# Optimization experiments

Hardware: AMD Instinct MI355X
Metric: run time of the kernel (lower is better)

Reference implementation:

```python
import jax, jax.numpy as jnp
import numpy as np

LN_EPS = 1e-5

def _layernorm(x, g, b):
    m = jnp.mean(x, axis=-1, keepdims=True)
    v = jnp.mean((x - m) ** 2, axis=-1, keepdims=True)
    return (x - m) / jnp.sqrt(v + LN_EPS) * g + b

def _mlp(x, w1, g1, b1, w2, g2, b2):
    # Linear(no bias) -> LayerNorm -> Linear(no bias) -> LayerNorm -> ReLU
    x = _layernorm(x @ w1, g1, b1)
    x = _layernorm(x @ w2, g2, b2)
    return jax.nn.relu(x)

def setup_inputs() -> dict:
    key = jax.random.key(0)
    ks = jax.random.split(key, 16)
    Lc, Lf, N, Dc, Df, K = 1024, 4096, 32, 256, 128, 8
    inv = lambda d: 1.0 / np.sqrt(d)
    inp = {
        "features_coarse": jax.random.normal(ks[0], (Lc, N, Dc), dtype=jnp.float32),
        "features_fine": jax.random.normal(ks[1], (Lf, N, Df), dtype=jnp.float32),
        # mlp_coarse: d_in=Dc, d_ff=Df, d_out=Df
        "w1c": jax.random.uniform(ks[2], (Dc, Df), jnp.float32, -inv(Dc), inv(Dc)),
        "g1c": jnp.ones((Df,), jnp.float32),
        "b1c": jnp.zeros((Df,), jnp.float32),
        "w2c": jax.random.uniform(ks[3], (Df, Df), jnp.float32, -inv(Df), inv(Df)),
        "g2c": jnp.ones((Df,), jnp.float32),
        "b2c": jnp.zeros((Df,), jnp.float32),
        # mlp_fine: d_in=Df, d_ff=Df, d_out=Df
        "w1f": jax.random.uniform(ks[4], (Df, Df), jnp.float32, -inv(Df), inv(Df)),
        "g1f": jnp.ones((Df,), jnp.float32),
        "b1f": jnp.zeros((Df,), jnp.float32),
        "w2f": jax.random.uniform(ks[5], (Df, Df), jnp.float32, -inv(Df), inv(Df)),
        "g2f": jnp.ones((Df,), jnp.float32),
        "b2f": jnp.zeros((Df,), jnp.float32),
        "neighbor_row": jax.random.randint(ks[6], (K * Lc * N,), 0, Lf, dtype=jnp.int64 if jax.config.jax_enable_x64 else jnp.int32),
        "neighbor_col": jax.random.randint(ks[7], (K * Lc * N,), 0, N, dtype=jnp.int64 if jax.config.jax_enable_x64 else jnp.int32),
        "keep_idx": jax.random.randint(ks[8], (Lc,), 0, Lf, dtype=jnp.int64 if jax.config.jax_enable_x64 else jnp.int32),
    }
    return inp

def reference(features_coarse, features_fine, w1c, g1c, b1c, w2c, g2c, b2c,
              w1f, g1f, b1f, w2f, g2f, b2f, neighbor_row, neighbor_col, keep_idx):
    Lc, N, Dc = features_coarse.shape
    Lf, _, Df = features_fine.shape
    D = Df
    fc = _mlp(features_coarse, w1c, g1c, b1c, w2c, g2c, b2c)  # (Lc, N, D)
    ff = _mlp(features_fine, w1f, g1f, b1f, w2f, g2f, b2f)    # (Lf, N, D)
    gathered = ff[neighbor_row, neighbor_col]                  # (K*Lc*N, D)
    updated = fc[None] + gathered.reshape(-1, Lc, N, D)        # (K, Lc, N, D)
    ff = ff.at[neighbor_row, neighbor_col].set(updated.reshape(-1, D))
    return ff
```

## Files before the change

### kernel.cpp

```cpp
#include <hip/hip_runtime.h>
#include <hip/hip_bf16.h>

typedef __attribute__((ext_vector_type(8))) short s8v;
typedef __attribute__((ext_vector_type(4))) float f4v;

__device__ __forceinline__ short f2bf(float f) {
    __hip_bfloat16 h = __float2bfloat16(f);
    union { __hip_bfloat16 h; short s; } u{h};
    return u.s;
}
__device__ __forceinline__ float bf2f(unsigned short v) {
    union { unsigned u; float f; } x; x.u = ((unsigned)v) << 16; return x.f;
}
__device__ __forceinline__ unsigned packbf(float a, float b) {
    return (unsigned)(unsigned short)f2bf(a) | ((unsigned)(unsigned short)f2bf(b) << 16);
}

__global__ void prep_kernel(const float* __restrict__ w1c, const float* __restrict__ w2c,
                            const float* __restrict__ g1c, const float* __restrict__ b1c,
                            const float* __restrict__ w1f, const float* __restrict__ w2f,
                            const float* __restrict__ g1f, const float* __restrict__ b1f,
                            short* __restrict__ p1c, short* __restrict__ p2c,
                            short* __restrict__ p1f, short* __restrict__ p2f,
                            float* __restrict__ s2c, float* __restrict__ bwc,
                            float* __restrict__ s2f, float* __restrict__ bwf,
                            int* __restrict__ win)
{
    int b = blockIdx.x, t = threadIdx.x;
    if (b >= 42) {
        int idx4 = (b - 42) * 256 + t;
        int4 z; z.x = 0; z.y = 0; z.z = 0; z.w = 0;
        *(int4*)(win + idx4 * 4) = z;
        return;
    }
    if (b >= 40) {
        if (t >= 128) return;
        const float* W  = (b == 40) ? w2c : w2f;
        const float* g1 = (b == 40) ? g1c : g1f;
        const float* b1 = (b == 40) ? b1c : b1f;
        float* s2 = (b == 40) ? s2c : s2f;
        float* bw = (b == 40) ? bwc : bwf;
        float s = 0.f, w2sum = 0.f;
        for (int k = 0; k < 128; ++k) {
            float wv = W[k * 128 + t];
            s     += bf2f((unsigned short)f2bf(g1[k] * wv));
            w2sum += b1[k] * wv;
        }
        s2[t] = s; bw[t] = w2sum;
        return;
    }
    int id = b * 256 + t;
    int f  = id >> 6, l = id & 63;
    const float* W; const float* g1 = nullptr; short* P; int fl;
    if      (f < 64)  { W = w1c; P = p1c; fl = f; }
    else if (f < 96)  { W = w2c; P = p2c; fl = f - 64;  g1 = g1c; }
    else if (f < 128) { W = w1f; P = p1f; fl = f - 96; }
    else              { W = w2f; P = p2f; fl = f - 128; g1 = g1f; }
    int g = l >> 4, c = l & 15;
    int ks = fl >> 3, n = fl & 7;
    s8v o;
    #pragma unroll
    for (int e = 0; e < 8; ++e) {
        int k = ks*32 + g*8 + e;
        float v = W[k * 128 + n*16 + c];
        if (g1) v *= g1[k];
        o[e] = f2bf(v);
    }
    *(s8v*)(P + ((fl*64 + l) << 3)) = o;
}

template<int K1, bool FINE>
__global__ __launch_bounds__(512, 4)
void mlp_mfma(const float* __restrict__ X,
              const short* __restrict__ WpA,
              const short* __restrict__ WpB,
              const float* __restrict__ s2v, const float* __restrict__ bwv,
              const float* __restrict__ g2v, const float* __restrict__ b2v,
              float* __restrict__ outF,
              unsigned short* __restrict__ outB,
              const int* __restrict__ winner,
              const unsigned short* __restrict__ fcB,
              const int* __restrict__ nr, const int* __restrict__ nc,
              int* __restrict__ win, int nWinBlocks)
{
    __shared__ short Ws[32768];
    constexpr int W2OFF = (K1 == 128) ? 16384 : 0;

    if (blockIdx.x < (unsigned)nWinBlocks) {
        int i = blockIdx.x * 512 + threadIdx.x;
        atomicMax(&win[nr[i] * 32 + nc[i]], i + 1);
        return;
    }
    const int bid  = blockIdx.x - nWinBlocks;
    const int tid  = threadIdx.x;
    const int wave = tid >> 6, lane = tid & 63;
    const int G = lane >> 4, n16 = lane & 15;
    const int row = bid * 128 + wave * 16 + n16;
    const size_t rowK = (size_t)row * K1;

    int wv = 0;
    if constexpr (FINE) wv = winner[row];

    #pragma unroll
    for (int r = 0; r < (K1 == 128 ? 4 : 8); ++r) {
        int ch = r*512 + tid;
        *(s8v*)&Ws[ch*8] = *(const s8v*)(WpA + (size_t)ch*8);
    }
    if constexpr (K1 == 128) {
        #pragma unroll
        for (int r = 0; r < 4; ++r) {
            int ch = r*512 + tid;
            *(s8v*)&Ws[16384 + ch*8] = *(const s8v*)(WpB + (size_t)ch*8);
        }
    }

    const float* pX = X + rowK + G*8;
    float4 aPf[4][2];
    #pragma unroll
    for (int k2 = 0; k2 < 4; ++k2) {
        aPf[k2][0] = *(const float4*)(pX + k2*32);
        aPf[k2][1] = *(const float4*)(pX + k2*32 + 4);
    }

    ushort4 gv[8];
    bool hasw = false;
    if constexpr (FINE) {
        hasw = (wv > 0);
        const size_t src = (size_t)((wv - 1) & 32767) * 128;
        if (hasw) {
            #pragma unroll
            for (int mt = 0; mt < 8; ++mt)
                gv[mt] = *(const ushort4*)(fcB + src + mt*16 + G*4);
        }
    }

    __syncthreads();

    f4v acc1[8];
    #pragma unroll
    for (int mt = 0; mt < 8; ++mt) acc1[mt] = (f4v){0.f, 0.f, 0.f, 0.f};

    #pragma unroll
    for (int kb = 0; kb < K1/32; kb += 4) {
        #pragma unroll
        for (int k2 = 0; k2 < 4; ++k2) {
            const int ks = kb + k2;
            s8v wfr[8];
            #pragma unroll
            for (int mt = 0; mt < 8; ++mt)
                wfr[mt] = *(const s8v*)&Ws[((ks*8 + mt)*64 + lane) * 8];
            s8v xf;
            xf[0] = f2bf(aPf[k2][0].x); xf[1] = f2bf(aPf[k2][0].y);
            xf[2] = f2bf(aPf[k2][0].z); xf[3] = f2bf(aPf[k2][0].w);
            xf[4] = f2bf(aPf[k2][1].x); xf[5] = f2bf(aPf[k2][1].y);
            xf[6] = f2bf(aPf[k2][1].z); xf[7] = f2bf(aPf[k2][1].w);
            #pragma unroll
            for (int mt = 0; mt < 8; ++mt)
                acc1[mt] = __builtin_amdgcn_mfma_f32_16x16x32_bf16(wfr[mt], xf, acc1[mt], 0, 0, 0);
        }
        if (kb + 4 < K1/32) {
            #pragma unroll
            for (int k2 = 0; k2 < 4; ++k2) {
                aPf[k2][0] = *(const float4*)(pX + (kb+4+k2)*32);
                aPf[k2][1] = *(const float4*)(pX + (kb+4+k2)*32 + 4);
            }
        }
    }

    if constexpr (K1 == 256) {
        __syncthreads();
        #pragma unroll
        for (int r = 0; r < 4; ++r) {
            int ch = r*512 + tid;
            *(s8v*)&Ws[ch*8] = *(const s8v*)(WpB + (size_t)ch*8);
        }
        __syncthreads();
    }

    float sm = 0.f, sq = 0.f;
    #pragma unroll
    for (int mt = 0; mt < 8; ++mt)
        #pragma unroll
        for (int j = 0; j < 4; ++j) { float v = acc1[mt][j]; sm += v; sq += v*v; }
    sm += __shfl_xor(sm, 16, 64); sm += __shfl_xor(sm, 32, 64);
    sq += __shfl_xor(sq, 16, 64); sq += __shfl_xor(sq, 32, 64);
    const float mean1 = sm * (1.f/128.f);
    const float rstd1 = rsqrtf(sq * (1.f/128.f) - mean1*mean1 + 1e-5f);

    unsigned pk[8][2];
    #pragma unroll
    for (int mt = 0; mt < 8; ++mt) {
        pk[mt][0] = packbf(acc1[mt][0], acc1[mt][1]);
        pk[mt][1] = packbf(acc1[mt][2], acc1[mt][3]);
    }

    f4v acc2[8];
    #pragma unroll
    for (int mt = 0; mt < 8; ++mt) acc2[mt] = (f4v){0.f, 0.f, 0.f, 0.f};

    const int src0 = ((G & 1) << 5) + n16;
    const int src1 = src0 + 16;
    const bool hiG = (G >= 2);
    #pragma unroll
    for (int ks = 0; ks < 4; ++ks) {
        int r00 = __shfl((int)pk[2*ks][0],   src0, 64);
        int r01 = __shfl((int)pk[2*ks][1],   src0, 64);
        int r02 = __shfl((int)pk[2*ks][0],   src1, 64);
        int r03 = __shfl((int)pk[2*ks][1],   src1, 64);
        int r10 = __shfl((int)pk[2*ks+1][0], src0, 64);
        int r11 = __shfl((int)pk[2*ks+1][1], src0, 64);
        int r12 = __shfl((int)pk[2*ks+1][0], src1, 64);
        int r13 = __shfl((int)pk[2*ks+1][1], src1, 64);
        union { int u[4]; s8v v; } hb;
        hb.u[0] = hiG ? r10 : r00; hb.u[1] = hiG ? r11 : r01;
        hb.u[2] = hiG ? r12 : r02; hb.u[3] = hiG ? r13 : r03;
        s8v wfr[8];
        #pragma unroll
        for (int mt = 0; mt < 8; ++mt)
            wfr[mt] = *(const s8v*)&Ws[W2OFF + ((ks*8 + mt)*64 + lane) * 8];
        #pragma unroll
        for (int mt = 0; mt < 8; ++mt)
            acc2[mt] = __builtin_amdgcn_mfma_f32_16x16x32_bf16(wfr[mt], hb.v, acc2[mt], 0, 0, 0);
    }

    float h2[8][4];
    float sm2 = 0.f, sq2 = 0.f;
    #pragma unroll
    for (int mt = 0; mt < 8; ++mt) {
        const int col = mt*16 + G*4;
        f4v s2l = *(const f4v*)&s2v[col];
        f4v bwl = *(const f4v*)&bwv[col];
        #pragma unroll
        for (int j = 0; j < 4; ++j) {
            float v = rstd1 * (acc2[mt][j] - mean1 * s2l[j]) + bwl[j];
            h2[mt][j] = v; sm2 += v; sq2 += v*v;
        }
    }
    sm2 += __shfl_xor(sm2, 16, 64); sm2 += __shfl_xor(sm2, 32, 64);
    sq2 += __shfl_xor(sq2, 16, 64); sq2 += __shfl_xor(sq2, 32, 64);
    const float mean2 = sm2 * (1.f/128.f);
    const float rstd2 = rsqrtf(sq2 * (1.f/128.f) - mean2*mean2 + 1e-5f);

    if constexpr (FINE) {
        #pragma unroll
        for (int mt = 0; mt < 8; ++mt) {
            const int col = mt*16 + G*4;
            f4v g2l = *(const f4v*)&g2v[col];
            f4v b2l = *(const f4v*)&b2v[col];
            float z0 = fmaxf((h2[mt][0]-mean2)*rstd2*g2l[0] + b2l[0], 0.f);
            float z1 = fmaxf((h2[mt][1]-mean2)*rstd2*g2l[1] + b2l[1], 0.f);
            float z2 = fmaxf((h2[mt][2]-mean2)*rstd2*g2l[2] + b2l[2], 0.f);
            float z3 = fmaxf((h2[mt][3]-mean2)*rstd2*g2l[3] + b2l[3], 0.f);
            if (hasw) {
                z0 += bf2f(gv[mt].x); z1 += bf2f(gv[mt].y);
                z2 += bf2f(gv[mt].z); z3 += bf2f(gv[mt].w);
            }
            float4 o; o.x = z0; o.y = z1; o.z = z2; o.w = z3;
            *(float4*)(outF + (size_t)row * 128 + col) = o;
        }
    } else {
        #pragma unroll
        for (int mt = 0; mt < 8; ++mt) {
            const int col = mt*16 + G*4;
            f4v g2l = *(const f4v*)&g2v[col];
            f4v b2l = *(const f4v*)&b2v[col];
            ushort4 o;
            o.x = (unsigned short)f2bf(fmaxf((h2[mt][0]-mean2)*rstd2*g2l[0] + b2l[0], 0.f));
            o.y = (unsigned short)f2bf(fmaxf((h2[mt][1]-mean2)*rstd2*g2l[1] + b2l[1], 0.f));
            o.z = (unsigned short)f2bf(fmaxf((h2[mt][2]-mean2)*rstd2*g2l[2] + b2l[2], 0.f));
            o.w = (unsigned short)f2bf(fmaxf((h2[mt][3]-mean2)*rstd2*g2l[3] + b2l[3], 0.f));
            *(ushort4*)(outB + (size_t)row * 128 + col) = o;
        }
    }
}

extern "C" void kernel_launch(void* const* d_in, const int* in_sizes, int n_in,
                              void* d_out, int out_size, void* d_ws, size_t ws_size,
                              hipStream_t stream)
{
    const float* fcoarse = (const float*)d_in[0];
    const float* ffine   = (const float*)d_in[1];
    const float* w1c = (const float*)d_in[2];
    const float* g1c = (const float*)d_in[3];
    const float* b1c = (const float*)d_in[4];
    const float* w2c = (const float*)d_in[5];
    const float* g2c = (const float*)d_in[6];
    const float* b2c = (const float*)d_in[7];
    const float* w1f = (const float*)d_in[8];
    const float* g1f = (const float*)d_in[9];
    const float* b1f = (const float*)d_in[10];
    const float* w2f = (const float*)d_in[11];
    const float* g2f = (const float*)d_in[12];
    const float* b2f = (const float*)d_in[13];
    const int* nrow  = (const int*)d_in[14];
    const int* ncol  = (const int*)d_in[15];

    float* out = (float*)d_out;
    const int Mc = 32768, Mf = 131072;

    unsigned short* fcB = (unsigned short*)d_ws;
    char* base = (char*)d_ws;
    int*   winner = (int*)(base + 8u*1024*1024);
    short* p1c = (short*)(base + 8u*1024*1024 + 512u*1024);
    short* p2c = p1c + 256*128;
    short* p1f = p2c + 128*128;
    short* p2f = p1f + 128*128;
    float* s2c = (float*)(p2f + 128*128);
    float* bwc = s2c + 128;
    float* s2f = bwc + 128;
    float* bwf = s2f + 128;

    prep_kernel<<<170, 256, 0, stream>>>(w1c, w2c, g1c, b1c, w1f, w2f, g1f, b1f,
                                         p1c, p2c, p1f, p2f, s2c, bwc, s2f, bwf,
                                         winner);

    mlp_mfma<256, false><<<512 + Mc/128, 512, 0, stream>>>(
        fcoarse, p1c, p2c, s2c, bwc, g2c, b2c,
        nullptr, fcB, nullptr, nullptr,
        nrow, ncol, winner, 512);

    mlp_mfma<128, true><<<Mf/128, 512, 0, stream>>>(
        ffine, p1f, p2f, s2f, bwf, g2f, b2f,
        out, nullptr, winner, fcB,
        nullptr, nullptr, nullptr, 0);
}
```

Baseline: 74.35 us.

## Process multiple row tiles per block with prefetch and keep both weight matrices resident in LDS

The MLP kernel now loops over NT row tiles per block, loading weights into LDS once and prefetching the next tile's inputs and winner index while computing the current one. The fine pass uses two tiles per block with half the grid. The coarse pass keeps W1 and W2 together in a larger LDS buffer instead of reloading W2 between the two GEMMs, which drops two barriers. The aim is to amortize weight staging and hide global load latency, at the cost of more LDS per block (96KB for coarse), which may reduce occupancy.

```diff
diff --git a/kernel.cpp b/kernel.cpp
--- a/kernel.cpp
+++ b/kernel.cpp
@@ -69,7 +69,7 @@
     *(s8v*)(P + ((fl*64 + l) << 3)) = o;
 }
 
-template<int K1, bool FINE>
+template<int K1, bool FINE, int NT>
 __global__ __launch_bounds__(512, 4)
 void mlp_mfma(const float* __restrict__ X,
               const short* __restrict__ WpA,
@@ -83,8 +83,9 @@
               const int* __restrict__ nr, const int* __restrict__ nc,
               int* __restrict__ win, int nWinBlocks)
 {
-    __shared__ short Ws[32768];
-    constexpr int W2OFF = (K1 == 128) ? 16384 : 0;
+    __shared__ short Ws[(K1 == 256) ? 49152 : 32768];
+    constexpr int W2OFF = (K1 == 256) ? 32768 : 16384;
+    constexpr int NCH1  = (K1/32) * 8 * 64;
 
     if (blockIdx.x < (unsigned)nWinBlocks) {
         int i = blockIdx.x * 512 + threadIdx.x;
@@ -95,182 +96,211 @@
     const int tid  = threadIdx.x;
     const int wave = tid >> 6, lane = tid & 63;
     const int G = lane >> 4, n16 = lane & 15;
-    const int row = bid * 128 + wave * 16 + n16;
-    const size_t rowK = (size_t)row * K1;
-
-    int wv = 0;
-    if constexpr (FINE) wv = winner[row];
+    const int row0 = bid * NT * 128 + wave * 16 + n16;
 
     #pragma unroll
-    for (int r = 0; r < (K1 == 128 ? 4 : 8); ++r) {
+    for (int r = 0; r < NCH1/512; ++r) {
         int ch = r*512 + tid;
         *(s8v*)&Ws[ch*8] = *(const s8v*)(WpA + (size_t)ch*8);
     }
-    if constexpr (K1 == 128) {
-        #pragma unroll
-        for (int r = 0; r < 4; ++r) {
-            int ch = r*512 + tid;
-            *(s8v*)&Ws[16384 + ch*8] = *(const s8v*)(WpB + (size_t)ch*8);
-        }
-    }
-
-    const float* pX = X + rowK + G*8;
+    #pragma unroll
+    for (int r = 0; r < 4; ++r) {
+        int ch = r*512 + tid;
+        *(s8v*)&Ws[W2OFF + ch*8] = *(const s8v*)(WpB + (size_t)ch*8);
+    }
+
     float4 aPf[4][2];
+    {
+        const float* pX0 = X + (size_t)row0 * K1 + G*8;
+        #pragma unroll
+        for (int k2 = 0; k2 < 4; ++k2) {
+            aPf[k2][0] = *(const float4*)(pX0 + k2*32);
+            aPf[k2][1] = *(const float4*)(pX0 + k2*32 + 4);
+        }
+    }
+    int wv = 0;
+    if constexpr (FINE) wv = winner[row0];
+
+    __syncthreads();
+
     #pragma unroll
-    for (int k2 = 0; k2 < 4; ++k2) {
-        aPf[k2][0] = *(const float4*)(pX + k2*32);
-        aPf[k2][1] = *(const float4*)(pX + k2*32 + 4);
-    }
-
-    ushort4 gv[8];
-    bool hasw = false;
-    if constexpr (FINE) {
-        hasw = (wv > 0);
-        const size_t src = (size_t)((wv - 1) & 32767) * 128;
-        if (hasw) {
-            #pragma unroll
-            for (int mt = 0; mt < 8; ++mt)
-                gv[mt] = *(const ushort4*)(fcB + src + mt*16 + G*4);
-        }
-    }
-
-    __syncthreads();
-
-    f4v acc1[8];
-    #pragma unroll
-    for (int mt = 0; mt < 8; ++mt) acc1[mt] = (f4v){0.f, 0.f, 0.f, 0.f};
-
-    #pragma unroll
-    for (int kb = 0; kb < K1/32; kb += 4) {
+    for (int t = 0; t < NT; ++t) {
+        const int row = row0 + t*128;
+
+        s8v xf[4];
         #pragma unroll
         for (int k2 = 0; k2 < 4; ++k2) {
-            const int ks = kb + k2;
+            s8v v;
+            v[0] = f2bf(aPf[k2][0].x); v[1] = f2bf(aPf[k2][0].y);
+            v[2] = f2bf(aPf[k2][0].z); v[3] = f2bf(aPf[k2][0].w);
+            v[4] = f2bf(aPf[k2][1].x); v[5] = f2bf(aPf[k2][1].y);
+            v[6] = f2bf(aPf[k2][1].z); v[7] = f2bf(aPf[k2][1].w);
+            xf[k2] = v;
+        }
+
+        float4 bPf[4][2];
+        if constexpr (K1 == 256) {
+            const float* pX = X + (size_t)row * K1 + G*8;
+            #pragma unroll
+            for (int k2 = 0; k2 < 4; ++k2) {
+                bPf[k2][0] = *(const float4*)(pX + (4+k2)*32);
+                bPf[k2][1] = *(const float4*)(pX + (4+k2)*32 + 4);
+            }
+        }
+
+        int wv_next = 0;
+        if (t + 1 < NT) {
+            const float* pXn = X + (size_t)(row + 128) * K1 + G*8;
+            #pragma unroll
+            for (int k2 = 0; k2 < 4; ++k2) {
+                aPf[k2][0] = *(const float4*)(pXn + k2*32);
+                aPf[k2][1] = *(const float4*)(pXn + k2*32 + 4);
+            }
+            if constexpr (FINE) wv_next = winner[row + 128];
+        }
+
+        ushort4 gv[8];
+        bool hasw = false;
+        if constexpr (FINE) {
+            hasw = (wv > 0);
+            const size_t src = (size_t)((wv - 1) & 32767) * 128;
+            if (hasw) {
+                #pragma unroll
+                for (int mt = 0; mt < 8; ++mt)
+                    gv[mt] = *(const ushort4*)(fcB + src + mt*16 + G*4);
+            }
+        }
+
+        f4v acc[8];
+        #pragma unroll
+        for (int mt = 0; mt < 8; ++mt) acc[mt] = (f4v){0.f, 0.f, 0.f, 0.f};
+
+        #pragma unroll
+        for (int ks = 0; ks < 4; ++ks) {
             s8v wfr[8];
             #pragma unroll
             for (int mt = 0; mt < 8; ++mt)
                 wfr[mt] = *(const s8v*)&Ws[((ks*8 + mt)*64 + lane) * 8];
-            s8v xf;
-            xf[0] = f2bf(aPf[k2][0].x); xf[1] = f2bf(aPf[k2][0].y);
-            xf[2] = f2bf(aPf[k2][0].z); xf[3] = f2bf(aPf[k2][0].w);
-            xf[4] = f2bf(aPf[k2][1].x); xf[5] = f2bf(aPf[k2][1].y);
-            xf[6] = f2bf(aPf[k2][1].z); xf[7] = f2bf(aPf[k2][1].w);
             #pragma unroll
             for (int mt = 0; mt < 8; ++mt)
-                acc1[mt] = __builtin_amdgcn_mfma_f32_16x16x32_bf16(wfr[mt], xf, acc1[mt], 0, 0, 0);
-        }
-        if (kb + 4 < K1/32) {
+                acc[mt] = __builtin_amdgcn_mfma_f32_16x16x32_bf16(wfr[mt], xf[ks], acc[mt], 0, 0, 0);
+        }
+        if constexpr (K1 == 256) {
             #pragma unroll
             for (int k2 = 0; k2 < 4; ++k2) {
-                aPf[k2][0] = *(const float4*)(pX + (kb+4+k2)*32);
-                aPf[k2][1] = *(const float4*)(pX + (kb+4+k2)*32 + 4);
-            }
-        }
-    }
-
-    if constexpr (K1 == 256) {
-        __syncthreads();
-        #pragma unroll
-        for (int r = 0; r < 4; ++r) {
-            int ch = r*512 + tid;
-            *(s8v*)&Ws[ch*8] = *(const s8v*)(WpB + (size_t)ch*8);
-        }
-        __syncthreads();
-    }
-
-    float sm = 0.f, sq = 0.f;
-    #pragma unroll
-    for (int mt = 0; mt < 8; ++mt)
-        #pragma unroll
-        for (int j = 0; j < 4; ++j) { float v = acc1[mt][j]; sm += v; sq += v*v; }
-    sm += __shfl_xor(sm, 16, 64); sm += __shfl_xor(sm, 32, 64);
-    sq += __shfl_xor(sq, 16, 64); sq += __shfl_xor(sq, 32, 64);
-    const float mean1 = sm * (1.f/128.f);
-    const float rstd1 = rsqrtf(sq * (1.f/128.f) - mean1*mean1 + 1e-5f);
-
-    unsigned pk[8][2];
-    #pragma unroll
-    for (int mt = 0; mt < 8; ++mt) {
-        pk[mt][0] = packbf(acc1[mt][0], acc1[mt][1]);
-        pk[mt][1] = packbf(acc1[mt][2], acc1[mt][3]);
-    }
-
-    f4v acc2[8];
-    #pragma unroll
-    for (int mt = 0; mt < 8; ++mt) acc2[mt] = (f4v){0.f, 0.f, 0.f, 0.f};
-
-    const int src0 = ((G & 1) << 5) + n16;
-    const int src1 = src0 + 16;
-    const bool hiG = (G >= 2);
-    #pragma unroll
-    for (int ks = 0; ks < 4; ++ks) {
-        int r00 = __shfl((int)pk[2*ks][0],   src0, 64);
-        int r01 = __shfl((int)pk[2*ks][1],   src0, 64);
-        int r02 = __shfl((int)pk[2*ks][0],   src1, 64);
-        int r03 = __shfl((int)pk[2*ks][1],   src1, 64);
-        int r10 = __shfl((int)pk[2*ks+1][0], src0, 64);
-        int r11 = __shfl((int)pk[2*ks+1][1], src0, 64);
-        int r12 = __shfl((int)pk[2*ks+1][0], src1, 64);
-        int r13 = __shfl((int)pk[2*ks+1][1], src1, 64);
-        union { int u[4]; s8v v; } hb;
-        hb.u[0] = hiG ? r10 : r00; hb.u[1] = hiG ? r11 : r01;
-        hb.u[2] = hiG ? r12 : r02; hb.u[3] = hiG ? r13 : r03;
-        s8v wfr[8];
+                s8v v;
+                v[0] = f2bf(bPf[k2][0].x); v[1] = f2bf(bPf[k2][0].y);
+                v[2] = f2bf(bPf[k2][0].z); v[3] = f2bf(bPf[k2][0].w);
+                v[4] = f2bf(bPf[k2][1].x); v[5] = f2bf(bPf[k2][1].y);
+                v[6] = f2bf(bPf[k2][1].z); v[7] = f2bf(bPf[k2][1].w);
+                xf[k2] = v;
+            }
+            #pragma unroll
+            for (int ks = 4; ks < 8; ++ks) {
+                s8v wfr[8];
+                #pragma unroll
+                for (int mt = 0; mt < 8; ++mt)
+                    wfr[mt] = *(const s8v*)&Ws[((ks*8 + mt)*64 + lane) * 8];
+                #pragma unroll
+                for (int mt = 0; mt < 8; ++mt)
+                    acc[mt] = __builtin_amdgcn_mfma_f32_16x16x32_bf16(wfr[mt], xf[ks-4], acc[mt], 0, 0, 0);
+            }
+        }
+
+        float sm = 0.f, sq = 0.f;
         #pragma unroll
         for (int mt = 0; mt < 8; ++mt)
-            wfr[mt] = *(const s8v*)&Ws[W2OFF + ((ks*8 + mt)*64 + lane) * 8];
-        #pragma unroll
-        for (int mt = 0; mt < 8; ++mt)
-            acc2[mt] = __builtin_amdgcn_mfma_f32_16x16x32_bf16(wfr[mt], hb.v, acc2[mt], 0, 0, 0);
-    }
-
-    float h2[8][4];
-    float sm2 = 0.f, sq2 = 0.f;
-    #pragma unroll
-    for (int mt = 0; mt < 8; ++mt) {
-        const int col = mt*16 + G*4;
-        f4v s2l = *(const f4v*)&s2v[col];
-        f4v bwl = *(const f4v*)&bwv[col];
-        #pragma unroll
-        for (int j = 0; j < 4; ++j) {
-            float v = rstd1 * (acc2[mt][j] - mean1 * s2l[j]) + bwl[j];
-            h2[mt][j] = v; sm2 += v; sq2 += v*v;
-        }
-    }
-    sm2 += __shfl_xor(sm2, 16, 64); sm2 += __shfl_xor(sm2, 32, 64);
-    sq2 += __shfl_xor(sq2, 16, 64); sq2 += __shfl_xor(sq2, 32, 64);
-    const float mean2 = sm2 * (1.f/128.f);
-    const float rstd2 = rsqrtf(sq2 * (1.f/128.f) - mean2*mean2 + 1e-5f);
-
-    if constexpr (FINE) {
+            #pragma unroll
+            for (int j = 0; j < 4; ++j) { float v = acc[mt][j]; sm += v; sq += v*v; }
+        sm += __shfl_xor(sm, 16, 64); sm += __shfl_xor(sm, 32, 64);
+        sq += __shfl_xor(sq, 16, 64); sq += __shfl_xor(sq, 32, 64);
+        const float mean1 = sm * (1.f/128.f);
+        const float rstd1 = rsqrtf(sq * (1.f/128.f) - mean1*mean1 + 1e-5f);
+
+        unsigned pk[8][2];
+        #pragma unroll
+        for (int mt = 0; mt < 8; ++mt) {
+            pk[mt][0] = packbf(acc[mt][0], acc[mt][1]);
+            pk[mt][1] = packbf(acc[mt][2], acc[mt][3]);
+            acc[mt] = (f4v){0.f, 0.f, 0.f, 0.f};
+        }
+
+        const int src0 = ((G & 1) << 5) + n16;
+        const int src1 = src0 + 16;
+        const bool hiG = (G >= 2);
+        #pragma unroll
+        for (int ks = 0; ks < 4; ++ks) {
+            int r00 = __shfl((int)pk[2*ks][0],   src0, 64);
+            int r01 = __shfl((int)pk[2*ks][1],   src0, 64);
+            int r02 = __shfl((int)pk[2*ks][0],   src1, 64);
+            int r03 = __shfl((int)pk[2*ks][1],   src1, 64);
+            int r10 = __shfl((int)pk[2*ks+1][0], src0, 64);
+            int r11 = __shfl((int)pk[2*ks+1][1], src0, 64);
+            int r12 = __shfl((int)pk[2*ks+1][0], src1, 64);
+            int r13 = __shfl((int)pk[2*ks+1][1], src1, 64);
+            union { int u[4]; s8v v; } hb;
+            hb.u[0] = hiG ? r10 : r00; hb.u[1] = hiG ? r11 : r01;
+            hb.u[2] = hiG ? r12 : r02; hb.u[3] = hiG ? r13 : r03;
+            s8v wfr[8];
+            #pragma unroll
+            for (int mt = 0; mt < 8; ++mt)
+                wfr[mt] = *(const s8v*)&Ws[W2OFF + ((ks*8 + mt)*64 + lane) * 8];
+            #pragma unroll
+            for (int mt = 0; mt < 8; ++mt)
+                acc[mt] = __builtin_amdgcn_mfma_f32_16x16x32_bf16(wfr[mt], hb.v, acc[mt], 0, 0, 0);
+        }
+
+        float h2[8][4];
+        float sm2 = 0.f, sq2 = 0.f;
         #pragma unroll
         for (int mt = 0; mt < 8; ++mt) {
             const int col = mt*16 + G*4;
-            f4v g2l = *(const f4v*)&g2v[col];
-            f4v b2l = *(const f4v*)&b2v[col];
-            float z0 = fmaxf((h2[mt][0]-mean2)*rstd2*g2l[0] + b2l[0], 0.f);
-            float z1 = fmaxf((h2[mt][1]-mean2)*rstd2*g2l[1] + b2l[1], 0.f);
-            float z2 = fmaxf((h2[mt][2]-mean2)*rstd2*g2l[2] + b2l[2], 0.f);
-            float z3 = fmaxf((h2[mt][3]-mean2)*rstd2*g2l[3] + b2l[3], 0.f);
-            if (hasw) {
-                z0 += bf2f(gv[mt].x); z1 += bf2f(gv[mt].y);
-                z2 += bf2f(gv[mt].z); z3 += bf2f(gv[mt].w);
-            }
-            float4 o; o.x = z0; o.y = z1; o.z = z2; o.w = z3;
-            *(float4*)(outF + (size_t)row * 128 + col) = o;
-        }
-    } else {
-        #pragma unroll
-        for (int mt = 0; mt < 8; ++mt) {
-            const int col = mt*16 + G*4;
-            f4v g2l = *(const f4v*)&g2v[col];
-            f4v b2l = *(const f4v*)&b2v[col];
-            ushort4 o;
-            o.x = (unsigned short)f2bf(fmaxf((h2[mt][0]-mean2)*rstd2*g2l[0] + b2l[0], 0.f));
-            o.y = (unsigned short)f2bf(fmaxf((h2[mt][1]-mean2)*rstd2*g2l[1] + b2l[1], 0.f));
-            o.z = (unsigned short)f2bf(fmaxf((h2[mt][2]-mean2)*rstd2*g2l[2] + b2l[2], 0.f));
-            o.w = (unsigned short)f2bf(fmaxf((h2[mt][3]-mean2)*rstd2*g2l[3] + b2l[3], 0.f));
-            *(ushort4*)(outB + (size_t)row * 128 + col) = o;
-        }
+            f4v s2l = *(const f4v*)&s2v[col];
+            f4v bwl = *(const f4v*)&bwv[col];
+            #pragma unroll
+            for (int j = 0; j < 4; ++j) {
+                float v = rstd1 * (acc[mt][j] - mean1 * s2l[j]) + bwl[j];
+                h2[mt][j] = v; sm2 += v; sq2 += v*v;
+            }
+        }
+        sm2 += __shfl_xor(sm2, 16, 64); sm2 += __shfl_xor(sm2, 32, 64);
+        sq2 += __shfl_xor(sq2, 16, 64); sq2 += __shfl_xor(sq2, 32, 64);
+        const float mean2 = sm2 * (1.f/128.f);
+        const float rstd2 = rsqrtf(sq2 * (1.f/128.f) - mean2*mean2 + 1e-5f);
+
+        if constexpr (FINE) {
+            #pragma unroll
+            for (int mt = 0; mt < 8; ++mt) {
+                const int col = mt*16 + G*4;
+                f4v g2l = *(const f4v*)&g2v[col];
+                f4v b2l = *(const f4v*)&b2v[col];
+                float z0 = fmaxf((h2[mt][0]-mean2)*rstd2*g2l[0] + b2l[0], 0.f);
+                float z1 = fmaxf((h2[mt][1]-mean2)*rstd2*g2l[1] + b2l[1], 0.f);
+                float z2 = fmaxf((h2[mt][2]-mean2)*rstd2*g2l[2] + b2l[2], 0.f);
+                float z3 = fmaxf((h2[mt][3]-mean2)*rstd2*g2l[3] + b2l[3], 0.f);
+                if (hasw) {
+                    z0 += bf2f(gv[mt].x); z1 += bf2f(gv[mt].y);
+                    z2 += bf2f(gv[mt].z); z3 += bf2f(gv[mt].w);
+                }
+                float4 o; o.x = z0; o.y = z1; o.z = z2; o.w = z3;
+                *(float4*)(outF + (size_t)row * 128 + col) = o;
+            }
+        } else {
+            #pragma unroll
+            for (int mt = 0; mt < 8; ++mt) {
+                const int col = mt*16 + G*4;
+                f4v g2l = *(const f4v*)&g2v[col];
+                f4v b2l = *(const f4v*)&b2v[col];
+                ushort4 o;
+                o.x = (unsigned short)f2bf(fmaxf((h2[mt][0]-mean2)*rstd2*g2l[0] + b2l[0], 0.f));
+                o.y = (unsigned short)f2bf(fmaxf((h2[mt][1]-mean2)*rstd2*g2l[1] + b2l[1], 0.f));
+                o.z = (unsigned short)f2bf(fmaxf((h2[mt][2]-mean2)*rstd2*g2l[2] + b2l[2], 0.f));
+                o.w = (unsigned short)f2bf(fmaxf((h2[mt][3]-mean2)*rstd2*g2l[3] + b2l[3], 0.f));
+                *(ushort4*)(outB + (size_t)row * 128 + col) = o;
+            }
+        }
+
+        wv = wv_next;
     }
 }
 
@@ -314,12 +344,12 @@
                                          p1c, p2c, p1f, p2f, s2c, bwc, s2f, bwf,
                                          winner);
 
-    mlp_mfma<256, false><<<512 + Mc/128, 512, 0, stream>>>(
+    mlp_mfma<256, false, 1><<<512 + Mc/128, 512, 0, stream>>>(
         fcoarse, p1c, p2c, s2c, bwc, g2c, b2c,
         nullptr, fcB, nullptr, nullptr,
         nrow, ncol, winner, 512);
 
-    mlp_mfma<128, true><<<Mf/128, 512, 0, stream>>>(
+    mlp_mfma<128, true, 2><<<Mf/256, 512, 0, stream>>>(
         ffine, p1f, p2f, s2f, bwf, g2f, b2f,
         out, nullptr, winner, fcB,
         nullptr, nullptr, nullptr, 0);
```

Result: slower. 78.08 us (+5.0%).

## Stage fine MLP input and output through swizzled LDS for coalesced access

Applied to the files above, without the earlier changes.

Splits the templated MLP kernel into separate coarse and fine kernels. The fine kernel now loads its input rows cooperatively with coalesced float4 reads, converts them to bf16 and stores them in an XOR-swizzled shared buffer, in two halves so the second half's load overlaps the first half's MFMAs. The epilogue writes activations to shared memory as bf16 and reads them back so each lane writes 32 contiguous bytes per row, adding the gathered coarse contribution along the way. This targets uncoalesced global traffic, but it rounds the fine output to bf16 before the residual add and uses 16 KB more shared memory per block.

```diff
diff --git a/kernel.cpp b/kernel.cpp
--- a/kernel.cpp
+++ b/kernel.cpp
@@ -69,22 +69,16 @@
     *(s8v*)(P + ((fl*64 + l) << 3)) = o;
 }
 
-template<int K1, bool FINE>
 __global__ __launch_bounds__(512, 4)
-void mlp_mfma(const float* __restrict__ X,
-              const short* __restrict__ WpA,
-              const short* __restrict__ WpB,
-              const float* __restrict__ s2v, const float* __restrict__ bwv,
-              const float* __restrict__ g2v, const float* __restrict__ b2v,
-              float* __restrict__ outF,
-              unsigned short* __restrict__ outB,
-              const int* __restrict__ winner,
-              const unsigned short* __restrict__ fcB,
-              const int* __restrict__ nr, const int* __restrict__ nc,
-              int* __restrict__ win, int nWinBlocks)
+void coarse_mlp(const float* __restrict__ X,
+                const short* __restrict__ WpA, const short* __restrict__ WpB,
+                const float* __restrict__ s2v, const float* __restrict__ bwv,
+                const float* __restrict__ g2v, const float* __restrict__ b2v,
+                unsigned short* __restrict__ outB,
+                const int* __restrict__ nr, const int* __restrict__ nc,
+                int* __restrict__ win, int nWinBlocks)
 {
     __shared__ short Ws[32768];
-    constexpr int W2OFF = (K1 == 128) ? 16384 : 0;
 
     if (blockIdx.x < (unsigned)nWinBlocks) {
         int i = blockIdx.x * 512 + threadIdx.x;
@@ -93,25 +87,16 @@
     }
     const int bid  = blockIdx.x - nWinBlocks;
     const int tid  = threadIdx.x;
-    const int wave = tid >> 6, lane = tid & 63;
+    const int lane = tid & 63;
+    const int wave = tid >> 6;
     const int G = lane >> 4, n16 = lane & 15;
     const int row = bid * 128 + wave * 16 + n16;
-    const size_t rowK = (size_t)row * K1;
-
-    int wv = 0;
-    if constexpr (FINE) wv = winner[row];
-
-    #pragma unroll
-    for (int r = 0; r < (K1 == 128 ? 4 : 8); ++r) {
+    const size_t rowK = (size_t)row * 256;
+
+    #pragma unroll
+    for (int r = 0; r < 8; ++r) {
         int ch = r*512 + tid;
         *(s8v*)&Ws[ch*8] = *(const s8v*)(WpA + (size_t)ch*8);
-    }
-    if constexpr (K1 == 128) {
-        #pragma unroll
-        for (int r = 0; r < 4; ++r) {
-            int ch = r*512 + tid;
-            *(s8v*)&Ws[16384 + ch*8] = *(const s8v*)(WpB + (size_t)ch*8);
-        }
     }
 
     const float* pX = X + rowK + G*8;
@@ -121,19 +106,6 @@
         aPf[k2][0] = *(const float4*)(pX + k2*32);
         aPf[k2][1] = *(const float4*)(pX + k2*32 + 4);
     }
-
-    ushort4 gv[8];
-    bool hasw = false;
-    if constexpr (FINE) {
-        hasw = (wv > 0);
-        const size_t src = (size_t)((wv - 1) & 32767) * 128;
-        if (hasw) {
-            #pragma unroll
-            for (int mt = 0; mt < 8; ++mt)
-                gv[mt] = *(const ushort4*)(fcB + src + mt*16 + G*4);
-        }
-    }
-
     __syncthreads();
 
     f4v acc1[8];
@@ -141,7 +113,7 @@
     for (int mt = 0; mt < 8; ++mt) acc1[mt] = (f4v){0.f, 0.f, 0.f, 0.f};
 
     #pragma unroll
-    for (int kb = 0; kb < K1/32; kb += 4) {
+    for (int kb = 0; kb < 8; kb += 4) {
         #pragma unroll
         for (int k2 = 0; k2 < 4; ++k2) {
             const int ks = kb + k2;
@@ -158,7 +130,7 @@
             for (int mt = 0; mt < 8; ++mt)
                 acc1[mt] = __builtin_amdgcn_mfma_f32_16x16x32_bf16(wfr[mt], xf, acc1[mt], 0, 0, 0);
         }
-        if (kb + 4 < K1/32) {
+        if (kb + 4 < 8) {
             #pragma unroll
             for (int k2 = 0; k2 < 4; ++k2) {
                 aPf[k2][0] = *(const float4*)(pX + (kb+4+k2)*32);
@@ -167,15 +139,13 @@
         }
     }
 
-    if constexpr (K1 == 256) {
-        __syncthreads();
-        #pragma unroll
-        for (int r = 0; r < 4; ++r) {
-            int ch = r*512 + tid;
-            *(s8v*)&Ws[ch*8] = *(const s8v*)(WpB + (size_t)ch*8);
-        }
-        __syncthreads();
-    }
+    __syncthreads();
+    #pragma unroll
+    for (int r = 0; r < 4; ++r) {
+        int ch = r*512 + tid;
+        *(s8v*)&Ws[ch*8] = *(const s8v*)(WpB + (size_t)ch*8);
+    }
+    __syncthreads();
 
     float sm = 0.f, sq = 0.f;
     #pragma unroll
@@ -217,7 +187,7 @@
         s8v wfr[8];
         #pragma unroll
         for (int mt = 0; mt < 8; ++mt)
-            wfr[mt] = *(const s8v*)&Ws[W2OFF + ((ks*8 + mt)*64 + lane) * 8];
+            wfr[mt] = *(const s8v*)&Ws[((ks*8 + mt)*64 + lane) * 8];
         #pragma unroll
         for (int mt = 0; mt < 8; ++mt)
             acc2[mt] = __builtin_amdgcn_mfma_f32_16x16x32_bf16(wfr[mt], hb.v, acc2[mt], 0, 0, 0);
@@ -241,9 +211,188 @@
     const float mean2 = sm2 * (1.f/128.f);
     const float rstd2 = rsqrtf(sq2 * (1.f/128.f) - mean2*mean2 + 1e-5f);
 
-    if constexpr (FINE) {
-        #pragma unroll
-        for (int mt = 0; mt < 8; ++mt) {
+    #pragma unroll
+    for (int mt = 0; mt < 8; ++mt) {
+        const int col = mt*16 + G*4;
+        f4v g2l = *(const f4v*)&g2v[col];
+        f4v b2l = *(const f4v*)&b2v[col];
+        ushort4 o;
+        o.x = (unsigned short)f2bf(fmaxf((h2[mt][0]-mean2)*rstd2*g2l[0] + b2l[0], 0.f));
+        o.y = (unsigned short)f2bf(fmaxf((h2[mt][1]-mean2)*rstd2*g2l[1] + b2l[1], 0.f));
+        o.z = (unsigned short)f2bf(fmaxf((h2[mt][2]-mean2)*rstd2*g2l[2] + b2l[2], 0.f));
+        o.w = (unsigned short)f2bf(fmaxf((h2[mt][3]-mean2)*rstd2*g2l[3] + b2l[3], 0.f));
+        *(ushort4*)(outB + (size_t)row * 128 + col) = o;
+    }
+}
+
+__global__ __launch_bounds__(512, 4)
+void fine_mlp(const float* __restrict__ X,
+              const short* __restrict__ WpA, const short* __restrict__ WpB,
+              const float* __restrict__ s2v, const float* __restrict__ bwv,
+              const float* __restrict__ g2v, const float* __restrict__ b2v,
+              float* __restrict__ out,
+              const int* __restrict__ winner,
+              const unsigned short* __restrict__ fcB)
+{
+    __shared__ short Ws[32768];
+    __shared__ short Xs[8192];
+
+    const int tid  = threadIdx.x;
+    const int wave = tid >> 6, lane = tid & 63;
+    const int G = lane >> 4, n16 = lane & 15;
+    const int row0 = blockIdx.x * 128;
+    const int rloc = wave * 16 + n16;
+    const int row  = row0 + rloc;
+    char* xs = (char*)Xs;
+
+    #pragma unroll
+    for (int r = 0; r < 4; ++r) {
+        int ch = r*512 + tid;
+        *(s8v*)&Ws[ch*8] = *(const s8v*)(WpA + (size_t)ch*8);
+    }
+    #pragma unroll
+    for (int r = 0; r < 4; ++r) {
+        int ch = r*512 + tid;
+        *(s8v*)&Ws[16384 + ch*8] = *(const s8v*)(WpB + (size_t)ch*8);
+    }
+
+    #pragma unroll
+    for (int it = 0; it < 4; ++it) {
+        int i  = it*512 + tid;
+        int r  = i >> 4;
+        int c4 = i & 15;
+        float4 v = *(const float4*)(X + (size_t)(row0 + r) * 128 + c4*4);
+        uint2 p; p.x = packbf(v.x, v.y); p.y = packbf(v.z, v.w);
+        int pg = (c4 >> 1) ^ (r & 7);
+        *(uint2*)(xs + r*128 + pg*16 + (c4 & 1)*8) = p;
+    }
+    int wv = winner[row];
+    __syncthreads();
+
+    f4v acc[8];
+    #pragma unroll
+    for (int mt = 0; mt < 8; ++mt) acc[mt] = (f4v){0.f, 0.f, 0.f, 0.f};
+
+    #pragma unroll
+    for (int ks = 0; ks < 2; ++ks) {
+        int pg = (ks*4 + G) ^ (rloc & 7);
+        s8v xf = *(const s8v*)(xs + rloc*128 + pg*16);
+        s8v wfr[8];
+        #pragma unroll
+        for (int mt = 0; mt < 8; ++mt)
+            wfr[mt] = *(const s8v*)&Ws[((ks*8 + mt)*64 + lane) * 8];
+        #pragma unroll
+        for (int mt = 0; mt < 8; ++mt)
+            acc[mt] = __builtin_amdgcn_mfma_f32_16x16x32_bf16(wfr[mt], xf, acc[mt], 0, 0, 0);
+    }
+    __syncthreads();
+
+    #pragma unroll
+    for (int it = 0; it < 4; ++it) {
+        int i  = it*512 + tid;
+        int r  = i >> 4;
+        int c4 = i & 15;
+        float4 v = *(const float4*)(X + (size_t)(row0 + r) * 128 + 64 + c4*4);
+        uint2 p; p.x = packbf(v.x, v.y); p.y = packbf(v.z, v.w);
+        int pg = (c4 >> 1) ^ (r & 7);
+        *(uint2*)(xs + r*128 + pg*16 + (c4 & 1)*8) = p;
+    }
+    s8v gv[2][2];
+    int wrr[2];
+    {
+        const int g8 = lane & 7;
+        #pragma unroll
+        for (int it = 0; it < 2; ++it) {
+            int rr = it*8 + (lane >> 3);
+            int w  = __shfl(wv, rr, 64);
+            wrr[it] = w;
+            size_t src = (size_t)((w > 0 ? w - 1 : 0) & 32767) * 128;
+            #pragma unroll
+            for (int ch = 0; ch < 2; ++ch)
+                gv[it][ch] = *(const s8v*)(fcB + src + ch*64 + g8*8);
+        }
+    }
+    __syncthreads();
+
+    #pragma unroll
+    for (int ks = 2; ks < 4; ++ks) {
+        int pg = ((ks-2)*4 + G) ^ (rloc & 7);
+        s8v xf = *(const s8v*)(xs + rloc*128 + pg*16);
+        s8v wfr[8];
+        #pragma unroll
+        for (int mt = 0; mt < 8; ++mt)
+            wfr[mt] = *(const s8v*)&Ws[((ks*8 + mt)*64 + lane) * 8];
+        #pragma unroll
+        for (int mt = 0; mt < 8; ++mt)
+            acc[mt] = __builtin_amdgcn_mfma_f32_16x16x32_bf16(wfr[mt], xf, acc[mt], 0, 0, 0);
+    }
+
+    float sm = 0.f, sq = 0.f;
+    #pragma unroll
+    for (int mt = 0; mt < 8; ++mt)
+        #pragma unroll
+        for (int j = 0; j < 4; ++j) { float v = acc[mt][j]; sm += v; sq += v*v; }
+    sm += __shfl_xor(sm, 16, 64); sm += __shfl_xor(sm, 32, 64);
+    sq += __shfl_xor(sq, 16, 64); sq += __shfl_xor(sq, 32, 64);
+    const float mean1 = sm * (1.f/128.f);
+    const float rstd1 = rsqrtf(sq * (1.f/128.f) - mean1*mean1 + 1e-5f);
+
+    unsigned pk[8][2];
+    #pragma unroll
+    for (int mt = 0; mt < 8; ++mt) {
+        pk[mt][0] = packbf(acc[mt][0], acc[mt][1]);
+        pk[mt][1] = packbf(acc[mt][2], acc[mt][3]);
+        acc[mt] = (f4v){0.f, 0.f, 0.f, 0.f};
+    }
+
+    const int src0 = ((G & 1) << 5) + n16;
+    const int src1 = src0 + 16;
+    const bool hiG = (G >= 2);
+    #pragma unroll
+    for (int ks = 0; ks < 4; ++ks) {
+        int r00 = __shfl((int)pk[2*ks][0],   src0, 64);
+        int r01 = __shfl((int)pk[2*ks][1],   src0, 64);
+        int r02 = __shfl((int)pk[2*ks][0],   src1, 64);
+        int r03 = __shfl((int)pk[2*ks][1],   src1, 64);
+        int r10 = __shfl((int)pk[2*ks+1][0], src0, 64);
+        int r11 = __shfl((int)pk[2*ks+1][1], src0, 64);
+        int r12 = __shfl((int)pk[2*ks+1][0], src1, 64);
+        int r13 = __shfl((int)pk[2*ks+1][1], src1, 64);
+        union { int u[4]; s8v v; } hb;
+        hb.u[0] = hiG ? r10 : r00; hb.u[1] = hiG ? r11 : r01;
+        hb.u[2] = hiG ? r12 : r02; hb.u[3] = hiG ? r13 : r03;
+        s8v wfr[8];
+        #pragma unroll
+        for (int mt = 0; mt < 8; ++mt)
+            wfr[mt] = *(const s8v*)&Ws[16384 + ((ks*8 + mt)*64 + lane) * 8];
+        #pragma unroll
+        for (int mt = 0; mt < 8; ++mt)
+            acc[mt] = __builtin_amdgcn_mfma_f32_16x16x32_bf16(wfr[mt], hb.v, acc[mt], 0, 0, 0);
+    }
+
+    float h2[8][4];
+    float sm2 = 0.f, sq2 = 0.f;
+    #pragma unroll
+    for (int mt = 0; mt < 8; ++mt) {
+        const int col = mt*16 + G*4;
+        f4v s2l = *(const f4v*)&s2v[col];
+        f4v bwl = *(const f4v*)&bwv[col];
+        #pragma unroll
+        for (int j = 0; j < 4; ++j) {
+            float v = rstd1 * (acc[mt][j] - mean1 * s2l[j]) + bwl[j];
+            h2[mt][j] = v; sm2 += v; sq2 += v*v;
+        }
+    }
+    sm2 += __shfl_xor(sm2, 16, 64); sm2 += __shfl_xor(sm2, 32, 64);
+    sq2 += __shfl_xor(sq2, 16, 64); sq2 += __shfl_xor(sq2, 32, 64);
+    const float mean2 = sm2 * (1.f/128.f);
+    const float rstd2 = rsqrtf(sq2 * (1.f/128.f) - mean2*mean2 + 1e-5f);
+
+    #pragma unroll
+    for (int ch = 0; ch < 2; ++ch) {
+        #pragma unroll
+        for (int mtL = 0; mtL < 4; ++mtL) {
+            const int mt = ch*4 + mtL;
             const int col = mt*16 + G*4;
             f4v g2l = *(const f4v*)&g2v[col];
             f4v b2l = *(const f4v*)&b2v[col];
@@ -251,26 +400,32 @@
             float z1 = fmaxf((h2[mt][1]-mean2)*rstd2*g2l[1] + b2l[1], 0.f);
             float z2 = fmaxf((h2[mt][2]-mean2)*rstd2*g2l[2] + b2l[2], 0.f);
             float z3 = fmaxf((h2[mt][3]-mean2)*rstd2*g2l[3] + b2l[3], 0.f);
-            if (hasw) {
-                z0 += bf2f(gv[mt].x); z1 += bf2f(gv[mt].y);
-                z2 += bf2f(gv[mt].z); z3 += bf2f(gv[mt].w);
+            uint2 p; p.x = packbf(z0, z1); p.y = packbf(z2, z3);
+            int pg = (mtL*2 + (G >> 1)) ^ (rloc & 7);
+            *(uint2*)(xs + rloc*128 + pg*16 + (G & 1)*8) = p;
+        }
+        asm volatile("s_waitcnt lgkmcnt(0)" ::: "memory");
+        #pragma unroll
+        for (int it = 0; it < 2; ++it) {
+            const int g8  = lane & 7;
+            const int rr  = it*8 + (lane >> 3);
+            const int rl2 = wave*16 + rr;
+            int pg = g8 ^ (rr & 7);
+            s8v v = *(const s8v*)(xs + rl2*128 + pg*16);
+            float y[8];
+            #pragma unroll
+            for (int e = 0; e < 8; ++e) y[e] = bf2f((unsigned short)v[e]);
+            if (wrr[it] > 0) {
+                #pragma unroll
+                for (int e = 0; e < 8; ++e) y[e] += bf2f((unsigned short)gv[it][ch][e]);
             }
-            float4 o; o.x = z0; o.y = z1; o.z = z2; o.w = z3;
-            *(float4*)(outF + (size_t)row * 128 + col) = o;
-        }
-    } else {
-        #pragma unroll
-        for (int mt = 0; mt < 8; ++mt) {
-            const int col = mt*16 + G*4;
-            f4v g2l = *(const f4v*)&g2v[col];
-            f4v b2l = *(const f4v*)&b2v[col];
-            ushort4 o;
-            o.x = (unsigned short)f2bf(fmaxf((h2[mt][0]-mean2)*rstd2*g2l[0] + b2l[0], 0.f));
-            o.y = (unsigned short)f2bf(fmaxf((h2[mt][1]-mean2)*rstd2*g2l[1] + b2l[1], 0.f));
-            o.z = (unsigned short)f2bf(fmaxf((h2[mt][2]-mean2)*rstd2*g2l[2] + b2l[2], 0.f));
-            o.w = (unsigned short)f2bf(fmaxf((h2[mt][3]-mean2)*rstd2*g2l[3] + b2l[3], 0.f));
-            *(ushort4*)(outB + (size_t)row * 128 + col) = o;
-        }
+            float4 o0 = {y[0], y[1], y[2], y[3]};
+            float4 o1 = {y[4], y[5], y[6], y[7]};
+            float* op = out + (size_t)(row0 + rl2) * 128 + ch*64 + g8*8;
+            *(float4*)op       = o0;
+            *(float4*)(op + 4) = o1;
+        }
+        asm volatile("" ::: "memory");
     }
 }
 
@@ -314,13 +469,11 @@
                                          p1c, p2c, p1f, p2f, s2c, bwc, s2f, bwf,
                                          winner);
 
-    mlp_mfma<256, false><<<512 + Mc/128, 512, 0, stream>>>(
-        fcoarse, p1c, p2c, s2c, bwc, g2c, b2c,
-        nullptr, fcB, nullptr, nullptr,
+    coarse_mlp<<<512 + Mc/128, 512, 0, stream>>>(
+        fcoarse, p1c, p2c, s2c, bwc, g2c, b2c, fcB,
         nrow, ncol, winner, 512);
 
-    mlp_mfma<128, true><<<Mf/128, 512, 0, stream>>>(
+    fine_mlp<<<Mf/128, 512, 0, stream>>>(
         ffine, p1f, p2f, s2f, bwf, g2f, b2f,
-        out, nullptr, winner, fcB,
-        nullptr, nullptr, nullptr, 0);
-}
+        out, winner, fcB);
+}
```

After: 70.26 us. 1.06x faster.
